# Kernel optimization log

Measured on AMD Instinct MI355X. Metric: run time of the kernel, lower is better.

The kernel has to match this reference:

```python
import jax, jax.numpy as jnp
import numpy as np

BITS = 8
CLIP_RATIO = 1.0
MAX_Q = 2 ** (BITS - 1) - 1  # 127
MIN_Q = -(MAX_Q + 1)         # -128


def setup_inputs() -> dict:
    key = jax.random.key(0)
    k1, k2, k3 = jax.random.split(key, 3)
    B, S, K, N = 4, 4096, 2048, 2048
    x = jax.random.normal(k1, (B, S, K), dtype=jnp.float32)
    # learned int8 weight [out_features, in_features] and per-row scale [out_features, 1]
    weight = jax.random.randint(k2, (N, K), MIN_Q, MAX_Q + 1, dtype=jnp.int32).astype(jnp.int8)
    weight_scale = jax.random.uniform(k3, (N, 1), dtype=jnp.float32, minval=1e-3, maxval=1e-2)
    return {"x": x, "weight": weight, "weight_scale": weight_scale}


def _quantize_sym(x):
    # per-token symmetric int8 quantization over the last dim
    mag = jnp.max(jnp.abs(x), axis=-1, keepdims=True) * CLIP_RATIO  # [B,S,1]
    scale = jnp.where(mag == 0, jnp.ones_like(mag), mag / MAX_Q)
    q = jnp.round(jnp.clip(x / scale, MIN_Q, MAX_Q)).astype(jnp.int8)
    return q, scale


def reference(x, weight, weight_scale):
    a, a_s = _quantize_sym(x)  # a: [B,S,K] int8, a_s: [B,S,1] f32
    res = jnp.einsum(
        'bsk,nk->bsn',
        a.astype(jnp.int32), weight.astype(jnp.int32),
    )  # [B,S,N] int32
    # dequantize: activation scale (per token) * weight scale (per out-channel)
    out = (res.astype(jnp.float32) * a_s * weight_scale.T).astype(x.dtype)
    return out
```

## Files before the change

### kernel.cpp

```cpp
#include <hip/hip_runtime.h>
#include <stdint.h>

#define M_DIM 16384
#define N_DIM 2048
#define K_DIM 2048

#define BM 256
#define BN 256
#define BK 64
#define NT (K_DIM / BK)
#define TILE_A_BYTES (BM * BK)
#define TILE_B_BYTES (BN * BK)
#define BUF_BYTES (TILE_A_BYTES + TILE_B_BYTES)
#define SMEM_BYTES (4 * BUF_BYTES)

typedef int v4i __attribute__((ext_vector_type(4)));

__global__ __launch_bounds__(256) void pack_w_kernel(const int* __restrict__ w32,
                                                     int8_t* __restrict__ w8) {
    const int i = (blockIdx.x * 256 + threadIdx.x) * 8;
    const int4 a = *reinterpret_cast<const int4*>(w32 + i);
    const int4 b = *reinterpret_cast<const int4*>(w32 + i + 4);
    uint32_t lo = (a.x & 255) | ((a.y & 255) << 8) | ((a.z & 255) << 16) | ((uint32_t)(a.w & 255) << 24);
    uint32_t hi = (b.x & 255) | ((b.y & 255) << 8) | ((b.z & 255) << 16) | ((uint32_t)(b.w & 255) << 24);
    int2 pk;
    pk.x = (int)lo;
    pk.y = (int)hi;
    *reinterpret_cast<int2*>(w8 + i) = pk;
}

__global__ __launch_bounds__(256) void quant_kernel(const float* __restrict__ x,
                                                    int8_t* __restrict__ q,
                                                    float* __restrict__ a_s) {
    const int row = blockIdx.x;
    const int t = threadIdx.x;
    const int lane = t & 63;
    const int wid = t >> 6;

    const float4* xv = reinterpret_cast<const float4*>(x + (size_t)row * K_DIM);
    float4 v0 = xv[t * 2 + 0];
    float4 v1 = xv[t * 2 + 1];

    float m = fmaxf(fmaxf(fmaxf(fabsf(v0.x), fabsf(v0.y)), fmaxf(fabsf(v0.z), fabsf(v0.w))),
                    fmaxf(fmaxf(fabsf(v1.x), fabsf(v1.y)), fmaxf(fabsf(v1.z), fabsf(v1.w))));

    #pragma unroll
    for (int off = 32; off > 0; off >>= 1)
        m = fmaxf(m, __shfl_xor(m, off));

    __shared__ float wmax[4];
    if (lane == 0) wmax[wid] = m;
    __syncthreads();
    const float mag = fmaxf(fmaxf(wmax[0], wmax[1]), fmaxf(wmax[2], wmax[3]));

    const float inv = (mag == 0.0f) ? 1.0f : (127.0f / mag);

    float e[8] = {v0.x, v0.y, v0.z, v0.w, v1.x, v1.y, v1.z, v1.w};
    uint32_t lo = 0, hi = 0;
    #pragma unroll
    for (int j = 0; j < 4; ++j) {
        float d = e[j] * inv;
        d = fminf(fmaxf(d, -128.0f), 127.0f);
        int qi = (int)rintf(d);
        lo |= ((uint32_t)(qi & 255)) << (8 * j);
    }
    #pragma unroll
    for (int j = 0; j < 4; ++j) {
        float d = e[4 + j] * inv;
        d = fminf(fmaxf(d, -128.0f), 127.0f);
        int qi = (int)rintf(d);
        hi |= ((uint32_t)(qi & 255)) << (8 * j);
    }

    int2 pk;
    pk.x = (int)lo;
    pk.y = (int)hi;
    reinterpret_cast<int2*>(q + (size_t)row * K_DIM)[t] = pk;

    if (t == 0) a_s[row] = (mag == 0.0f) ? 1.0f : (mag / 127.0f);
}

__global__ __launch_bounds__(512, 2) void gemm_i8_kernel(
    const int8_t* __restrict__ A,
    const int8_t* __restrict__ W,
    const float* __restrict__ a_s,
    const float* __restrict__ w_s,
    float* __restrict__ out)
{
    extern __shared__ int8_t smem[];

    const int t = threadIdx.x;
    const int lane = t & 63;
    const int wid = t >> 6;
    const int wr = wid >> 2;
    const int wc = wid & 3;

    const int bid = blockIdx.x;
    const int sbid = (bid & 7) * (gridDim.x >> 3) + (bid >> 3);
    const int bm = sbid >> 3;
    const int bn = sbid & 7;

    const int8_t* aSrc = A + (size_t)(bm * BM) * K_DIM;
    const int8_t* bSrc = W + (size_t)(bn * BN) * K_DIM;

    const int f0 = t, f1 = t + 512;
    const int r0 = f0 >> 2, u0 = f0 & 3;
    const int r1 = f1 >> 2, u1 = f1 & 3;
    const size_t gOff0 = (size_t)r0 * K_DIM + (size_t)((u0 ^ ((r0 >> 1) & 3)) << 4);
    const size_t gOff1 = (size_t)r1 * K_DIM + (size_t)((u1 ^ ((r1 >> 1) & 3)) << 4);

    #define STAGE(tile)                                                                     \
    do {                                                                                    \
        int8_t* base_ = smem + ((tile) & 3) * BUF_BYTES;                                    \
        const int k0_ = (tile) * BK;                                                        \
        __builtin_amdgcn_global_load_lds(                                                   \
            (const __attribute__((address_space(1))) void*)(aSrc + k0_ + gOff0),            \
            (__attribute__((address_space(3))) void*)(base_ + f0 * 16), 16, 0, 0);          \
        __builtin_amdgcn_global_load_lds(                                                   \
            (const __attribute__((address_space(1))) void*)(aSrc + k0_ + gOff1),            \
            (__attribute__((address_space(3))) void*)(base_ + f1 * 16), 16, 0, 0);          \
        __builtin_amdgcn_global_load_lds(                                                   \
            (const __attribute__((address_space(1))) void*)(bSrc + k0_ + gOff0),            \
            (__attribute__((address_space(3))) void*)(base_ + TILE_A_BYTES + f0 * 16), 16, 0, 0); \
        __builtin_amdgcn_global_load_lds(                                                   \
            (const __attribute__((address_space(1))) void*)(bSrc + k0_ + gOff1),            \
            (__attribute__((address_space(3))) void*)(base_ + TILE_A_BYTES + f1 * 16), 16, 0, 0); \
    } while (0)

    const int frow = lane & 15;
    const int fc = lane >> 4;
    const int rA = wr * 128 + frow;
    const int rB = wc * 64 + frow;
    const int aOff = rA * 64 + ((((rA >> 1) & 3) ^ fc) << 4);
    const int bOff = rB * 64 + ((((rB >> 1) & 3) ^ fc) << 4);

    v4i acc[8][4] = {};

    STAGE(0);
    STAGE(1);
    STAGE(2);
    asm volatile("s_waitcnt vmcnt(8)" ::: "memory");
    __builtin_amdgcn_s_barrier();
    asm volatile("" ::: "memory");

    for (int tt = 0; tt < NT; ++tt) {
        if (tt + 3 < NT) STAGE(tt + 3);

        const int8_t* Ab = smem + (tt & 3) * BUF_BYTES;
        const int8_t* Bb = Ab + TILE_A_BYTES;

        v4i af[8], bf[4];
        #pragma unroll
        for (int mf = 0; mf < 8; ++mf)
            af[mf] = *(const v4i*)(Ab + aOff + mf * 1024);
        #pragma unroll
        for (int nf = 0; nf < 4; ++nf)
            bf[nf] = *(const v4i*)(Bb + bOff + nf * 1024);

        __builtin_amdgcn_s_setprio(1);
        #pragma unroll
        for (int mf = 0; mf < 8; ++mf)
            #pragma unroll
            for (int nf = 0; nf < 4; ++nf)
                acc[mf][nf] = __builtin_amdgcn_mfma_i32_16x16x64_i8(
                    af[mf], bf[nf], acc[mf][nf], 0, 0, 0);
        __builtin_amdgcn_s_setprio(0);

        if (tt < NT - 1) {
            asm volatile("" ::: "memory");
            if (tt < NT - 3)        asm volatile("s_waitcnt vmcnt(8)" ::: "memory");
            else if (tt < NT - 2)   asm volatile("s_waitcnt vmcnt(4)" ::: "memory");
            else                    asm volatile("s_waitcnt vmcnt(0)" ::: "memory");
            __builtin_amdgcn_s_barrier();
            asm volatile("" ::: "memory");
        }
    }
    #undef STAGE

    const int row0 = bm * BM + wr * 128;
    const int col0 = bn * BN + wc * 64;
    #pragma unroll
    for (int mf = 0; mf < 8; ++mf) {
        const int rbase = row0 + mf * 16 + (lane >> 4) * 4;
        #pragma unroll
        for (int nf = 0; nf < 4; ++nf) {
            const int c = col0 + nf * 16 + (lane & 15);
            const float ws = w_s[c];
            #pragma unroll
            for (int j = 0; j < 4; ++j) {
                const int r = rbase + j;
                out[(size_t)r * N_DIM + c] = ((float)acc[mf][nf][j] * a_s[r]) * ws;
            }
        }
    }
}

extern "C" void kernel_launch(void* const* d_in, const int* in_sizes, int n_in,
                              void* d_out, int out_size, void* d_ws, size_t ws_size,
                              hipStream_t stream) {
    const float* x = (const float*)d_in[0];
    const int* w32 = (const int*)d_in[1];
    const float* wscale = (const float*)d_in[2];
    float* out = (float*)d_out;

    int8_t* q = (int8_t*)d_ws;
    float* a_s = (float*)((char*)d_ws + (size_t)M_DIM * K_DIM);
    int8_t* w8 = (int8_t*)((char*)d_ws + (size_t)M_DIM * K_DIM + (size_t)M_DIM * 4);

    static int smem_set = 0;
    if (!smem_set) {
        hipFuncSetAttribute(reinterpret_cast<const void*>(&gemm_i8_kernel),
                            hipFuncAttributeMaxDynamicSharedMemorySize, SMEM_BYTES);
        smem_set = 1;
    }

    pack_w_kernel<<<(N_DIM * K_DIM) / (256 * 8), 256, 0, stream>>>(w32, w8);
    quant_kernel<<<M_DIM, 256, 0, stream>>>(x, q, a_s);

    const int grid = (M_DIM / BM) * (N_DIM / BN);
    gemm_i8_kernel<<<grid, 512, SMEM_BYTES, stream>>>(q, w8, a_s, wscale, out);
}
```

Measured before the change: 309.0 us.

## Split GEMM k-step into two MFMA phases with interleaved staging; one-wave-per-row quant

The GEMM main loop is split into two halves. The A prefetch is issued after the first fragment loads and the B prefetch after the second A-fragment loads, with extra barriers around each MFMA phase, so global-to-LDS traffic is spread across the iteration and ping-pong style scheduling between waves is encouraged. The quantization kernel now maps one wavefront per row, which removes the LDS reduction and the block barrier. The added barriers per k-step could cost more than the better overlap gains.

Result: no change. 311.5 us (+0.8%).

```diff
diff --git a/kernel.cpp b/kernel.cpp
--- a/kernel.cpp
+++ b/kernel.cpp
@@ -32,52 +32,44 @@
 __global__ __launch_bounds__(256) void quant_kernel(const float* __restrict__ x,
                                                     int8_t* __restrict__ q,
                                                     float* __restrict__ a_s) {
-    const int row = blockIdx.x;
-    const int t = threadIdx.x;
-    const int lane = t & 63;
-    const int wid = t >> 6;
+    const int lane = threadIdx.x & 63;
+    const int wid = threadIdx.x >> 6;
+    const int row = blockIdx.x * 4 + wid;
 
     const float4* xv = reinterpret_cast<const float4*>(x + (size_t)row * K_DIM);
-    float4 v0 = xv[t * 2 + 0];
-    float4 v1 = xv[t * 2 + 1];
-
-    float m = fmaxf(fmaxf(fmaxf(fabsf(v0.x), fabsf(v0.y)), fmaxf(fabsf(v0.z), fabsf(v0.w))),
-                    fmaxf(fmaxf(fabsf(v1.x), fabsf(v1.y)), fmaxf(fabsf(v1.z), fabsf(v1.w))));
-
+    float4 v[8];
+    #pragma unroll
+    for (int j = 0; j < 8; ++j) v[j] = xv[lane + 64 * j];
+
+    float m = 0.0f;
+    #pragma unroll
+    for (int j = 0; j < 8; ++j) {
+        m = fmaxf(m, fmaxf(fmaxf(fabsf(v[j].x), fabsf(v[j].y)),
+                           fmaxf(fabsf(v[j].z), fabsf(v[j].w))));
+    }
     #pragma unroll
     for (int off = 32; off > 0; off >>= 1)
         m = fmaxf(m, __shfl_xor(m, off));
-
-    __shared__ float wmax[4];
-    if (lane == 0) wmax[wid] = m;
-    __syncthreads();
-    const float mag = fmaxf(fmaxf(wmax[0], wmax[1]), fmaxf(wmax[2], wmax[3]));
+    const float mag = m;
 
     const float inv = (mag == 0.0f) ? 1.0f : (127.0f / mag);
 
-    float e[8] = {v0.x, v0.y, v0.z, v0.w, v1.x, v1.y, v1.z, v1.w};
-    uint32_t lo = 0, hi = 0;
-    #pragma unroll
-    for (int j = 0; j < 4; ++j) {
-        float d = e[j] * inv;
-        d = fminf(fmaxf(d, -128.0f), 127.0f);
-        int qi = (int)rintf(d);
-        lo |= ((uint32_t)(qi & 255)) << (8 * j);
-    }
-    #pragma unroll
-    for (int j = 0; j < 4; ++j) {
-        float d = e[4 + j] * inv;
-        d = fminf(fmaxf(d, -128.0f), 127.0f);
-        int qi = (int)rintf(d);
-        hi |= ((uint32_t)(qi & 255)) << (8 * j);
-    }
-
-    int2 pk;
-    pk.x = (int)lo;
-    pk.y = (int)hi;
-    reinterpret_cast<int2*>(q + (size_t)row * K_DIM)[t] = pk;
-
-    if (t == 0) a_s[row] = (mag == 0.0f) ? 1.0f : (mag / 127.0f);
+    uint32_t* qo = reinterpret_cast<uint32_t*>(q + (size_t)row * K_DIM);
+    #pragma unroll
+    for (int j = 0; j < 8; ++j) {
+        float e[4] = {v[j].x, v[j].y, v[j].z, v[j].w};
+        uint32_t pk = 0;
+        #pragma unroll
+        for (int c = 0; c < 4; ++c) {
+            float d = e[c] * inv;
+            d = fminf(fmaxf(d, -128.0f), 127.0f);
+            int qi = (int)rintf(d);
+            pk |= ((uint32_t)(qi & 255)) << (8 * c);
+        }
+        qo[lane + 64 * j] = pk;
+    }
+
+    if (lane == 0) a_s[row] = (mag == 0.0f) ? 1.0f : (mag / 127.0f);
 }
 
 __global__ __launch_bounds__(512, 2) void gemm_i8_kernel(
@@ -109,7 +101,7 @@
     const size_t gOff0 = (size_t)r0 * K_DIM + (size_t)((u0 ^ ((r0 >> 1) & 3)) << 4);
     const size_t gOff1 = (size_t)r1 * K_DIM + (size_t)((u1 ^ ((r1 >> 1) & 3)) << 4);
 
-    #define STAGE(tile)                                                                     \
+    #define STAGE_A(tile)                                                                   \
     do {                                                                                    \
         int8_t* base_ = smem + ((tile) & 3) * BUF_BYTES;                                    \
         const int k0_ = (tile) * BK;                                                        \
@@ -119,12 +111,18 @@
         __builtin_amdgcn_global_load_lds(                                                   \
             (const __attribute__((address_space(1))) void*)(aSrc + k0_ + gOff1),            \
             (__attribute__((address_space(3))) void*)(base_ + f1 * 16), 16, 0, 0);          \
+    } while (0)
+
+    #define STAGE_B(tile)                                                                   \
+    do {                                                                                    \
+        int8_t* base_ = smem + ((tile) & 3) * BUF_BYTES + TILE_A_BYTES;                     \
+        const int k0_ = (tile) * BK;                                                        \
         __builtin_amdgcn_global_load_lds(                                                   \
             (const __attribute__((address_space(1))) void*)(bSrc + k0_ + gOff0),            \
-            (__attribute__((address_space(3))) void*)(base_ + TILE_A_BYTES + f0 * 16), 16, 0, 0); \
+            (__attribute__((address_space(3))) void*)(base_ + f0 * 16), 16, 0, 0);          \
         __builtin_amdgcn_global_load_lds(                                                   \
             (const __attribute__((address_space(1))) void*)(bSrc + k0_ + gOff1),            \
-            (__attribute__((address_space(3))) void*)(base_ + TILE_A_BYTES + f1 * 16), 16, 0, 0); \
+            (__attribute__((address_space(3))) void*)(base_ + f1 * 16), 16, 0, 0);          \
     } while (0)
 
     const int frow = lane & 15;
@@ -136,46 +134,73 @@
 
     v4i acc[8][4] = {};
 
-    STAGE(0);
-    STAGE(1);
-    STAGE(2);
+    STAGE_A(0); STAGE_B(0);
+    STAGE_A(1); STAGE_B(1);
+    STAGE_A(2); STAGE_B(2);
     asm volatile("s_waitcnt vmcnt(8)" ::: "memory");
     __builtin_amdgcn_s_barrier();
     asm volatile("" ::: "memory");
 
     for (int tt = 0; tt < NT; ++tt) {
-        if (tt + 3 < NT) STAGE(tt + 3);
-
         const int8_t* Ab = smem + (tt & 3) * BUF_BYTES;
         const int8_t* Bb = Ab + TILE_A_BYTES;
-
-        v4i af[8], bf[4];
-        #pragma unroll
-        for (int mf = 0; mf < 8; ++mf)
-            af[mf] = *(const v4i*)(Ab + aOff + mf * 1024);
+        const bool pf = (tt + 3 < NT);
+
+        v4i af0[4], bf[4];
+        #pragma unroll
+        for (int mf = 0; mf < 4; ++mf)
+            af0[mf] = *(const v4i*)(Ab + aOff + mf * 1024);
         #pragma unroll
         for (int nf = 0; nf < 4; ++nf)
             bf[nf] = *(const v4i*)(Bb + bOff + nf * 1024);
+        if (pf) STAGE_A(tt + 3);
+
+        asm volatile("" ::: "memory");
+        __builtin_amdgcn_s_barrier();
+        asm volatile("" ::: "memory");
 
         __builtin_amdgcn_s_setprio(1);
         #pragma unroll
-        for (int mf = 0; mf < 8; ++mf)
+        for (int mf = 0; mf < 4; ++mf)
             #pragma unroll
             for (int nf = 0; nf < 4; ++nf)
                 acc[mf][nf] = __builtin_amdgcn_mfma_i32_16x16x64_i8(
-                    af[mf], bf[nf], acc[mf][nf], 0, 0, 0);
+                    af0[mf], bf[nf], acc[mf][nf], 0, 0, 0);
         __builtin_amdgcn_s_setprio(0);
 
+        asm volatile("" ::: "memory");
+        __builtin_amdgcn_s_barrier();
+        asm volatile("" ::: "memory");
+
+        v4i af1[4];
+        #pragma unroll
+        for (int mf = 0; mf < 4; ++mf)
+            af1[mf] = *(const v4i*)(Ab + aOff + 4096 + mf * 1024);
+        if (pf) STAGE_B(tt + 3);
+
         if (tt < NT - 1) {
-            asm volatile("" ::: "memory");
-            if (tt < NT - 3)        asm volatile("s_waitcnt vmcnt(8)" ::: "memory");
-            else if (tt < NT - 2)   asm volatile("s_waitcnt vmcnt(4)" ::: "memory");
-            else                    asm volatile("s_waitcnt vmcnt(0)" ::: "memory");
-            __builtin_amdgcn_s_barrier();
-            asm volatile("" ::: "memory");
+            if (tt < NT - 3)      asm volatile("s_waitcnt vmcnt(8)" ::: "memory");
+            else if (tt < NT - 2) asm volatile("s_waitcnt vmcnt(4)" ::: "memory");
+            else                  asm volatile("s_waitcnt vmcnt(0)" ::: "memory");
         }
-    }
-    #undef STAGE
+        __builtin_amdgcn_s_barrier();
+        asm volatile("" ::: "memory");
+
+        __builtin_amdgcn_s_setprio(1);
+        #pragma unroll
+        for (int mf = 0; mf < 4; ++mf)
+            #pragma unroll
+            for (int nf = 0; nf < 4; ++nf)
+                acc[mf + 4][nf] = __builtin_amdgcn_mfma_i32_16x16x64_i8(
+                    af1[mf], bf[nf], acc[mf + 4][nf], 0, 0, 0);
+        __builtin_amdgcn_s_setprio(0);
+
+        asm volatile("" ::: "memory");
+        __builtin_amdgcn_s_barrier();
+        asm volatile("" ::: "memory");
+    }
+    #undef STAGE_A
+    #undef STAGE_B
 
     const int row0 = bm * BM + wr * 128;
     const int col0 = bn * BN + wc * 64;
@@ -215,7 +240,7 @@
     }
 
     pack_w_kernel<<<(N_DIM * K_DIM) / (256 * 8), 256, 0, stream>>>(w32, w8);
-    quant_kernel<<<M_DIM, 256, 0, stream>>>(x, q, a_s);
+    quant_kernel<<<M_DIM / 4, 256, 0, stream>>>(x, q, a_s);
 
     const int grid = (M_DIM / BM) * (N_DIM / BN);
     gemm_i8_kernel<<<grid, 512, SMEM_BYTES, stream>>>(q, w8, a_s, wscale, out);
```
